# Optimization experiments

Hardware: AMD Instinct MI355X
Metric: run time of the kernel (lower is better)

## Reference

```python
import jax, jax.numpy as jnp
import numpy as np

NBLOCK = 2000
DIM = 2048
B, T = 32, 1024
EPS = 1e-12  # F.normalize eps


def _l2norm(v, axis):
    n = jnp.sqrt(jnp.sum(v * v, axis=axis, keepdims=True))
    return v / jnp.maximum(n, EPS)


def setup_inputs() -> dict:
    key = jax.random.key(0)
    kx, km, kw = jax.random.split(key, 3)
    x = jax.random.normal(kx, (B, T, DIM), dtype=jnp.float32)
    mask = jax.random.randint(km, (B, T), 0, 2).astype(jnp.int32)
    stdv = 1.0 / np.sqrt(DIM)
    weight = jax.random.uniform(kw, (NBLOCK, DIM), dtype=jnp.float32,
                                minval=-stdv, maxval=stdv)
    return {"x": x, "mask": mask, "weight": weight}


def reference(x, mask, weight):
    half = x.shape[0] // 2
    nblock = weight.shape[0]
    m = mask.astype(x.dtype)  # [B, T]

    # diversity: || W W^T - I ||_F
    gram = weight @ weight.T  # [N, N]
    diversity_loss = jnp.linalg.norm(gram - jnp.eye(nblock, dtype=weight.dtype))

    # cosine-similarity attention: [B, T, N]
    att = jnp.einsum('btd,nd->btn', _l2norm(x, axis=2), _l2norm(weight, axis=1))

    # uniformity loss: masked sum over T, softmax over blocks, mean over half-batch
    s = jnp.einsum('btn,bt->nb', att[:half], m[:half])  # [N, half]
    tmp = jnp.mean(jax.nn.softmax(s, axis=0), axis=1)   # [N]
    u_loss = jnp.linalg.norm(tmp)

    # per-row min over masked positions of the top-1 similarity
    top1 = jnp.max(att, axis=2)  # [B, T] (only topk[...,0] is used)
    inf = jnp.asarray(jnp.inf, dtype=x.dtype)
    masked_top1 = jnp.where(m > 0, top1, inf)
    min_sim = jnp.min(masked_top1[:half], axis=1)   # [half]
    ab_min = jnp.min(masked_top1[half:], axis=1)    # [half]

    return (0.2 * diversity_loss,
            2.0 - jnp.mean(min_sim) + jnp.mean(ab_min),
            0.5 * u_loss)
```

## Files before the change

kernel.cpp:

```cpp
#include <hip/hip_runtime.h>

typedef unsigned short u16;
typedef unsigned int u32;
typedef __attribute__((ext_vector_type(8))) short short8;
typedef __attribute__((ext_vector_type(8))) u16 ushort8;
typedef __attribute__((ext_vector_type(4))) u16 ushort4_t;
typedef __attribute__((ext_vector_type(4))) float fx4;

#define DIMK 2048
#define NBLK 2000

typedef const __attribute__((address_space(1))) void* gp_t;
typedef __attribute__((address_space(3))) void* lp_t;

__device__ __forceinline__ u16 f2bf(float f) {
  u32 u = __float_as_uint(f);
  u32 r = (u + 0x7fffu + ((u >> 16) & 1u)) >> 16;
  return (u16)r;
}

__device__ __forceinline__ u32 fkey(float f) {
  u32 u = __float_as_uint(f);
  return (u & 0x80000000u) ? ~u : (u | 0x80000000u);
}
__device__ __forceinline__ float dekey(u32 k) {
  u32 u = (k & 0x80000000u) ? (k ^ 0x80000000u) : ~k;
  return __uint_as_float(u);
}

__device__ __forceinline__ void ring_gemm128(const u16* gA0, const u16* gA1,
                                             const u16* gB0, const u16* gB1,
                                             u16 (*ring)[2][4096],
                                             int wv, int wr, int wc, int fIntra,
                                             fx4 acc[4][4])
{
#pragma unroll
  for (int mi = 0; mi < 4; mi++)
#pragma unroll
    for (int ni = 0; ni < 4; ni++)
      acc[mi][ni] = fx4{0.f, 0.f, 0.f, 0.f};

#define STG(kt)                                                                  \
  do {                                                                           \
    const int ko_ = (kt) << 5;                                                   \
    u16* lA_ = &ring[(kt) % 3][0][wv << 10];                                     \
    u16* lB_ = &ring[(kt) % 3][1][wv << 10];                                     \
    __builtin_amdgcn_global_load_lds((gp_t)(gA0 + ko_), (lp_t)lA_,         16, 0, 0); \
    __builtin_amdgcn_global_load_lds((gp_t)(gA1 + ko_), (lp_t)(lA_ + 512), 16, 0, 0); \
    __builtin_amdgcn_global_load_lds((gp_t)(gB0 + ko_), (lp_t)lB_,         16, 0, 0); \
    __builtin_amdgcn_global_load_lds((gp_t)(gB1 + ko_), (lp_t)(lB_ + 512), 16, 0, 0); \
  } while (0)

  STG(0);
  STG(1);

  const int NT = DIMK / 32;
#pragma unroll 1
  for (int t = 0; t < NT; ++t) {
    if (t + 2 < NT) {
      STG(t + 2);
      asm volatile("s_waitcnt vmcnt(8)" ::: "memory");
    } else if (t + 1 < NT) {
      asm volatile("s_waitcnt vmcnt(4)" ::: "memory");
    } else {
      asm volatile("s_waitcnt vmcnt(0)" ::: "memory");
    }
    __builtin_amdgcn_s_barrier();

    const u16* lAt = &ring[t % 3][0][0];
    const u16* lBt = &ring[t % 3][1][0];
    short8 af[4], bfr[4];
#pragma unroll
    for (int ni = 0; ni < 4; ni++)
      bfr[ni] = *(const short8*)(lBt + (wc * 4 + ni) * 512 + fIntra);
#pragma unroll
    for (int mi = 0; mi < 4; mi++)
      af[mi] = *(const short8*)(lAt + (wr * 4 + mi) * 512 + fIntra);

    __builtin_amdgcn_s_setprio(1);
#pragma unroll
    for (int mi = 0; mi < 4; mi++)
#pragma unroll
      for (int ni = 0; ni < 4; ni++)
        acc[mi][ni] = __builtin_amdgcn_mfma_f32_16x16x32_bf16(af[mi], bfr[ni], acc[mi][ni], 0, 0, 0);
    __builtin_amdgcn_s_setprio(0);
    __builtin_amdgcn_s_barrier();
  }
#undef STG
}

__global__ __launch_bounds__(256) void norm_rows_x(const float* __restrict__ x,
                                                   u16* __restrict__ Xn)
{
  const int wv = threadIdx.x >> 6, lane = threadIdx.x & 63;
  const int row = blockIdx.x * 4 + wv;
  const float4* xr = (const float4*)(x + (size_t)row * DIMK);
  float4 v[8];
  float ss = 0.f;
#pragma unroll
  for (int j = 0; j < 8; j++) {
    v[j] = xr[j * 64 + lane];
    ss += v[j].x*v[j].x + v[j].y*v[j].y + v[j].z*v[j].z + v[j].w*v[j].w;
  }
#pragma unroll
  for (int off = 1; off < 64; off <<= 1) ss += __shfl_xor(ss, off);
  float inv = 1.0f / fmaxf(sqrtf(ss), 1e-12f);
  ushort4_t* o = (ushort4_t*)(Xn + (size_t)row * DIMK);
#pragma unroll
  for (int j = 0; j < 8; j++) {
    ushort4_t t;
    t[0] = f2bf(v[j].x * inv); t[1] = f2bf(v[j].y * inv);
    t[2] = f2bf(v[j].z * inv); t[3] = f2bf(v[j].w * inv);
    o[j * 64 + lane] = t;
  }
}

__global__ __launch_bounds__(256) void norm_rows_w(const float* __restrict__ w,
                                                   u16* __restrict__ Wn,
                                                   u16* __restrict__ Wb)
{
  const int wv = threadIdx.x >> 6, lane = threadIdx.x & 63;
  const int row = blockIdx.x * 4 + wv;
  ushort4_t* on_ = (ushort4_t*)(Wn + (size_t)row * DIMK);
  ushort4_t* ob_ = (ushort4_t*)(Wb + (size_t)row * DIMK);
  if (row < NBLK) {
    const float4* wr_ = (const float4*)(w + (size_t)row * DIMK);
    float4 v[8];
    float ss = 0.f;
#pragma unroll
    for (int j = 0; j < 8; j++) {
      v[j] = wr_[j * 64 + lane];
      ss += v[j].x*v[j].x + v[j].y*v[j].y + v[j].z*v[j].z + v[j].w*v[j].w;
    }
#pragma unroll
    for (int off = 1; off < 64; off <<= 1) ss += __shfl_xor(ss, off);
    float inv = 1.0f / fmaxf(sqrtf(ss), 1e-12f);
#pragma unroll
    for (int j = 0; j < 8; j++) {
      ushort4_t tn, tb;
      tn[0] = f2bf(v[j].x * inv); tn[1] = f2bf(v[j].y * inv);
      tn[2] = f2bf(v[j].z * inv); tn[3] = f2bf(v[j].w * inv);
      tb[0] = f2bf(v[j].x); tb[1] = f2bf(v[j].y);
      tb[2] = f2bf(v[j].z); tb[3] = f2bf(v[j].w);
      on_[j * 64 + lane] = tn;
      ob_[j * 64 + lane] = tb;
    }
  } else {
    ushort4_t z = ushort4_t{0, 0, 0, 0};
#pragma unroll
    for (int j = 0; j < 8; j++) { on_[j * 64 + lane] = z; ob_[j * 64 + lane] = z; }
  }
}

__global__ __launch_bounds__(256) void gram_kernel(const u16* __restrict__ Wb,
                                                   float* __restrict__ divsum)
{
  const int bx = blockIdx.x, by = blockIdx.y;
  if (by > bx) return;
  __shared__ __align__(16) u16 ring[3][2][4096];
  const int tid = threadIdx.x, wv = tid >> 6, lane = tid & 63;
  const int wr = wv & 1, wc = wv >> 1, quad = lane >> 4, lc = lane & 15;
  const int i0 = by * 128, j0 = bx * 128;

  const int srow = wv * 32 + (lane >> 2);
  const int skel = (((lane & 3) ^ ((lane >> 3) & 3)) << 3);
  const u16* gA0 = Wb + (size_t)(i0 + srow) * DIMK + skel;
  const u16* gA1 = gA0 + (size_t)16 * DIMK;
  const u16* gB0 = Wb + (size_t)(j0 + srow) * DIMK + skel;
  const u16* gB1 = gB0 + (size_t)16 * DIMK;
  const int fIntra = lc * 32 + ((quad ^ ((lc >> 1) & 3)) << 3);

  fx4 acc[4][4];
  ring_gemm128(gA0, gA1, gB0, gB1, ring, wv, wr, wc, fIntra, acc);

  const float mult = (bx == by) ? 1.0f : 2.0f;
  float local = 0.f;
#pragma unroll
  for (int mi = 0; mi < 4; mi++) {
#pragma unroll
    for (int ni = 0; ni < 4; ni++) {
#pragma unroll
      for (int r = 0; r < 4; r++) {
        int i = i0 + wr * 64 + mi * 16 + quad * 4 + r;
        int j = j0 + wc * 64 + ni * 16 + lc;
        float g = acc[mi][ni][r];
        float d = (i == j && i < NBLK) ? 1.0f : 0.0f;
        float e = g - d;
        local += e * e;
      }
    }
  }
  local *= mult;
#pragma unroll
  for (int off = 1; off < 64; off <<= 1) local += __shfl_xor(local, off);
  if (lane == 0) atomicAdd(divsum, local);
}

__global__ __launch_bounds__(256, 2) void att_kernel(const u16* __restrict__ Xn,
                                                     const u16* __restrict__ Wn,
                                                     const int* __restrict__ mask,
                                                     u32* __restrict__ top1k,
                                                     float* __restrict__ s)
{
  __shared__ __align__(16) u16 ring[3][12288];

  const int orig  = blockIdx.x;
  const int xcd   = orig & 7;
  const int local = orig >> 3;
  const int yb    = xcd * 32 + ((local >> 5) << 2) + (local & 3);
  const int xb    = (local >> 2) & 7;
  const int row0 = yb << 7, col0 = xb << 8;

  const int tid = threadIdx.x, wv = tid >> 6, lane = tid & 63;
  const int wr = wv >> 1, wc = wv & 1, quad = lane >> 4, lc = lane & 15;

  const int srow = lane >> 2;
  const int skel = (((lane & 3) ^ ((lane >> 3) & 3)) << 3);
  const u16* gA0 = Xn + (size_t)(row0 + wv * 32 + srow) * DIMK + skel;
  const u16* gA1 = gA0 + (size_t)16 * DIMK;
  const u16* gB0 = Wn + (size_t)(col0 + wv * 64 + srow) * DIMK + skel;
  const u16* gB1 = gB0 + (size_t)16 * DIMK;
  const u16* gB2 = gB0 + (size_t)32 * DIMK;
  const u16* gB3 = gB0 + (size_t)48 * DIMK;
  const int fIntra = lc * 32 + ((quad ^ ((lc >> 1) & 3)) << 3);

  fx4 acc[4][8];
#pragma unroll
  for (int mi = 0; mi < 4; mi++)
#pragma unroll
    for (int ni = 0; ni < 8; ni++)
      acc[mi][ni] = fx4{0.f, 0.f, 0.f, 0.f};

#define STG6(kt)                                                                 \
  do {                                                                           \
    const int ko_ = (kt) << 5;                                                   \
    u16* lA_ = &ring[(kt) % 3][wv << 10];                                        \
    u16* lB_ = &ring[(kt) % 3][4096 + (wv << 11)];                               \
    __builtin_amdgcn_global_load_lds((gp_t)(gA0 + ko_), (lp_t)lA_,          16, 0, 0); \
    __builtin_amdgcn_global_load_lds((gp_t)(gA1 + ko_), (lp_t)(lA_ + 512),  16, 0, 0); \
    __builtin_amdgcn_global_load_lds((gp_t)(gB0 + ko_), (lp_t)lB_,          16, 0, 0); \
    __builtin_amdgcn_global_load_lds((gp_t)(gB1 + ko_), (lp_t)(lB_ + 512),  16, 0, 0); \
    __builtin_amdgcn_global_load_lds((gp_t)(gB2 + ko_), (lp_t)(lB_ + 1024), 16, 0, 0); \
    __builtin_amdgcn_global_load_lds((gp_t)(gB3 + ko_), (lp_t)(lB_ + 1536), 16, 0, 0); \
  } while (0)

  STG6(0);
  STG6(1);

  const int NT = DIMK / 32;
#pragma unroll 1
  for (int t = 0; t < NT; ++t) {
    if (t + 2 < NT) {
      STG6(t + 2);
      asm volatile("s_waitcnt vmcnt(12)" ::: "memory");
    } else if (t + 1 < NT) {
      asm volatile("s_waitcnt vmcnt(6)" ::: "memory");
    } else {
      asm volatile("s_waitcnt vmcnt(0)" ::: "memory");
    }
    __builtin_amdgcn_s_barrier();

    const u16* lAt = &ring[t % 3][0];
    const u16* lBt = &ring[t % 3][0] + 4096;
    short8 af[4], bfr[8];
#pragma unroll
    for (int ni = 0; ni < 8; ni++)
      bfr[ni] = *(const short8*)(lBt + (wc * 8 + ni) * 512 + fIntra);
#pragma unroll
    for (int mi = 0; mi < 4; mi++)
      af[mi] = *(const short8*)(lAt + (wr * 4 + mi) * 512 + fIntra);

    __builtin_amdgcn_s_setprio(1);
#pragma unroll
    for (int mi = 0; mi < 4; mi++)
#pragma unroll
      for (int ni = 0; ni < 8; ni++)
        acc[mi][ni] = __builtin_amdgcn_mfma_f32_16x16x32_bf16(af[mi], bfr[ni], acc[mi][ni], 0, 0, 0);
    __builtin_amdgcn_s_setprio(0);
    __builtin_amdgcn_s_barrier();
  }
#undef STG6

#pragma unroll
  for (int mi = 0; mi < 4; mi++) {
#pragma unroll
    for (int r = 0; r < 4; r++) {
      float v = -3.0e38f;
#pragma unroll
      for (int ni = 0; ni < 8; ni++) {
        int col = col0 + wc * 128 + ni * 16 + lc;
        float av = acc[mi][ni][r];
        v = (col < NBLK && av > v) ? av : v;
      }
      v = fmaxf(v, __shfl_xor(v, 1));
      v = fmaxf(v, __shfl_xor(v, 2));
      v = fmaxf(v, __shfl_xor(v, 4));
      v = fmaxf(v, __shfl_xor(v, 8));
      if (lc == 0) {
        int row = row0 + wr * 64 + mi * 16 + quad * 4 + r;
        atomicMax(&top1k[row], fkey(v));
      }
    }
  }

  if (yb < 128) {
    const int b = yb >> 3;
    float sv[8] = {0.f, 0.f, 0.f, 0.f, 0.f, 0.f, 0.f, 0.f};
#pragma unroll
    for (int mi = 0; mi < 4; mi++) {
#pragma unroll
      for (int r = 0; r < 4; r++) {
        float mval = (float)mask[row0 + wr * 64 + mi * 16 + quad * 4 + r];
#pragma unroll
        for (int ni = 0; ni < 8; ni++)
          sv[ni] += mval * acc[mi][ni][r];
      }
    }
#pragma unroll
    for (int ni = 0; ni < 8; ni++) {
      float v = sv[ni];
      v += __shfl_xor(v, 16);
      v += __shfl_xor(v, 32);
      int col = col0 + wc * 128 + ni * 16 + lc;
      if (quad == 0 && col < NBLK)
        atomicAdd(&s[b * 2048 + col], v);
    }
  }
}

__global__ __launch_bounds__(1024) void tail_kernel(const float* __restrict__ s,
                                                    const u32* __restrict__ top1k,
                                                    const int* __restrict__ mask,
                                                    const float* __restrict__ divsum,
                                                    float* __restrict__ out)
{
  const int tid = threadIdx.x;
  const int w = tid >> 6, lane = tid & 63;
  __shared__ float mx_s[16], ise_s[16];
  __shared__ float red[16];
  __shared__ float sMin[32];

  const float* sb = s + w * 2048;
  float mx = -3.0e38f;
  for (int n = lane; n < NBLK; n += 64) mx = fmaxf(mx, sb[n]);
#pragma unroll
  for (int off = 1; off < 64; off <<= 1) mx = fmaxf(mx, __shfl_xor(mx, off));
  float se = 0.f;
  for (int n = lane; n < NBLK; n += 64) se += expf(sb[n] - mx);
#pragma unroll
  for (int off = 1; off < 64; off <<= 1) se += __shfl_xor(se, off);
  if (lane == 0) { mx_s[w] = mx; ise_s[w] = 1.0f / (se * 16.0f); }
  __syncthreads();

  float ssq = 0.f;
  for (int n = tid; n < NBLK; n += 1024) {
    float v = 0.f;
#pragma unroll
    for (int b = 0; b < 16; b++)
      v += expf(s[b * 2048 + n] - mx_s[b]) * ise_s[b];
    ssq += v * v;
  }
#pragma unroll
  for (int off = 1; off < 64; off <<= 1) ssq += __shfl_xor(ssq, off);
  if (lane == 0) red[w] = ssq;

  const int b = tid >> 5, li = tid & 31;
  float mn = 3.0e38f;
  for (int t = li; t < 1024; t += 32) {
    int idx = b * 1024 + t;
    if (mask[idx] > 0) mn = fminf(mn, dekey(top1k[idx]));
  }
#pragma unroll
  for (int off = 1; off < 32; off <<= 1) mn = fminf(mn, __shfl_xor(mn, off));
  if (li == 0) sMin[b] = mn;
  __syncthreads();

  if (tid == 0) {
    float m0 = 0.f, m1 = 0.f;
    for (int i = 0; i < 16; i++) { m0 += sMin[i]; m1 += sMin[16 + i]; }
    m0 *= (1.0f / 16.0f); m1 *= (1.0f / 16.0f);
    float sq = 0.f;
    for (int i = 0; i < 16; i++) sq += red[i];
    out[0] = 0.2f * sqrtf(divsum[0]);
    out[1] = 2.0f - m0 + m1;
    out[2] = 0.5f * sqrtf(sq);
  }
}

extern "C" void kernel_launch(void* const* d_in, const int* in_sizes, int n_in,
                              void* d_out, int out_size, void* d_ws, size_t ws_size,
                              hipStream_t stream) {
  const float* x    = (const float*)d_in[0];
  const int*   mask = (const int*)d_in[1];
  const float* w    = (const float*)d_in[2];
  float* out = (float*)d_out;

  char* ws = (char*)d_ws;
  u32*   top1k  = (u32*)(ws);
  float* s      = (float*)(ws + 131072);
  float* divsum = (float*)(ws + 270336);
  u16*   Xn     = (u16*)(ws + 270592);
  u16*   Wn     = (u16*)(ws + 270592 + 134217728ull);
  u16*   Wb     = (u16*)(ws + 270592 + 134217728ull + 8388608ull);

  hipMemsetAsync(ws, 0, 270592, stream);

  norm_rows_w<<<dim3(512), dim3(256), 0, stream>>>(w, Wn, Wb);
  norm_rows_x<<<dim3(8192), dim3(256), 0, stream>>>(x, Xn);
  gram_kernel<<<dim3(16, 16), dim3(256), 0, stream>>>(Wb, divsum);
  att_kernel<<<dim3(2048), dim3(256), 0, stream>>>(Xn, Wn, mask, top1k, s);
  tail_kernel<<<dim3(1), dim3(1024), 0, stream>>>(s, top1k, mask, divsum, out);
}
```

Measured before the change: 724.7 us.

## Replace LDS triple-buffered staging with direct global-to-register MFMA operand loads

Both GEMM kernels (gram and attention) drop the shared-memory ring buffer fed by global_load_lds, along with its waitcnt and barrier pipeline. Each wave now loads its MFMA A/B fragments straight from global memory into registers at every k-step. This removes LDS traffic, barriers and LDS occupancy limits. In exchange it loses data sharing across waves, so the same tiles are fetched multiple times through cache, and there is no explicit prefetch, leaving global latency exposed each iteration.

Measured after the change: 1.205 ms. 66.3% more time.

```diff
diff --git a/kernel.cpp b/kernel.cpp
--- a/kernel.cpp
+++ b/kernel.cpp
@@ -3,15 +3,11 @@
 typedef unsigned short u16;
 typedef unsigned int u32;
 typedef __attribute__((ext_vector_type(8))) short short8;
-typedef __attribute__((ext_vector_type(8))) u16 ushort8;
 typedef __attribute__((ext_vector_type(4))) u16 ushort4_t;
 typedef __attribute__((ext_vector_type(4))) float fx4;
 
 #define DIMK 2048
 #define NBLK 2000
-
-typedef const __attribute__((address_space(1))) void* gp_t;
-typedef __attribute__((address_space(3))) void* lp_t;
 
 __device__ __forceinline__ u16 f2bf(float f) {
   u32 u = __float_as_uint(f);
@@ -26,67 +22,6 @@
 __device__ __forceinline__ float dekey(u32 k) {
   u32 u = (k & 0x80000000u) ? (k ^ 0x80000000u) : ~k;
   return __uint_as_float(u);
-}
-
-__device__ __forceinline__ void ring_gemm128(const u16* gA0, const u16* gA1,
-                                             const u16* gB0, const u16* gB1,
-                                             u16 (*ring)[2][4096],
-                                             int wv, int wr, int wc, int fIntra,
-                                             fx4 acc[4][4])
-{
-#pragma unroll
-  for (int mi = 0; mi < 4; mi++)
-#pragma unroll
-    for (int ni = 0; ni < 4; ni++)
-      acc[mi][ni] = fx4{0.f, 0.f, 0.f, 0.f};
-
-#define STG(kt)                                                                  \
-  do {                                                                           \
-    const int ko_ = (kt) << 5;                                                   \
-    u16* lA_ = &ring[(kt) % 3][0][wv << 10];                                     \
-    u16* lB_ = &ring[(kt) % 3][1][wv << 10];                                     \
-    __builtin_amdgcn_global_load_lds((gp_t)(gA0 + ko_), (lp_t)lA_,         16, 0, 0); \
-    __builtin_amdgcn_global_load_lds((gp_t)(gA1 + ko_), (lp_t)(lA_ + 512), 16, 0, 0); \
-    __builtin_amdgcn_global_load_lds((gp_t)(gB0 + ko_), (lp_t)lB_,         16, 0, 0); \
-    __builtin_amdgcn_global_load_lds((gp_t)(gB1 + ko_), (lp_t)(lB_ + 512), 16, 0, 0); \
-  } while (0)
-
-  STG(0);
-  STG(1);
-
-  const int NT = DIMK / 32;
-#pragma unroll 1
-  for (int t = 0; t < NT; ++t) {
-    if (t + 2 < NT) {
-      STG(t + 2);
-      asm volatile("s_waitcnt vmcnt(8)" ::: "memory");
-    } else if (t + 1 < NT) {
-      asm volatile("s_waitcnt vmcnt(4)" ::: "memory");
-    } else {
-      asm volatile("s_waitcnt vmcnt(0)" ::: "memory");
-    }
-    __builtin_amdgcn_s_barrier();
-
-    const u16* lAt = &ring[t % 3][0][0];
-    const u16* lBt = &ring[t % 3][1][0];
-    short8 af[4], bfr[4];
-#pragma unroll
-    for (int ni = 0; ni < 4; ni++)
-      bfr[ni] = *(const short8*)(lBt + (wc * 4 + ni) * 512 + fIntra);
-#pragma unroll
-    for (int mi = 0; mi < 4; mi++)
-      af[mi] = *(const short8*)(lAt + (wr * 4 + mi) * 512 + fIntra);
-
-    __builtin_amdgcn_s_setprio(1);
-#pragma unroll
-    for (int mi = 0; mi < 4; mi++)
-#pragma unroll
-      for (int ni = 0; ni < 4; ni++)
-        acc[mi][ni] = __builtin_amdgcn_mfma_f32_16x16x32_bf16(af[mi], bfr[ni], acc[mi][ni], 0, 0, 0);
-    __builtin_amdgcn_s_setprio(0);
-    __builtin_amdgcn_s_barrier();
-  }
-#undef STG
 }
 
 __global__ __launch_bounds__(256) void norm_rows_x(const float* __restrict__ x,
@@ -157,21 +92,36 @@
 {
   const int bx = blockIdx.x, by = blockIdx.y;
   if (by > bx) return;
-  __shared__ __align__(16) u16 ring[3][2][4096];
   const int tid = threadIdx.x, wv = tid >> 6, lane = tid & 63;
   const int wr = wv & 1, wc = wv >> 1, quad = lane >> 4, lc = lane & 15;
   const int i0 = by * 128, j0 = bx * 128;
 
-  const int srow = wv * 32 + (lane >> 2);
-  const int skel = (((lane & 3) ^ ((lane >> 3) & 3)) << 3);
-  const u16* gA0 = Wb + (size_t)(i0 + srow) * DIMK + skel;
-  const u16* gA1 = gA0 + (size_t)16 * DIMK;
-  const u16* gB0 = Wb + (size_t)(j0 + srow) * DIMK + skel;
-  const u16* gB1 = gB0 + (size_t)16 * DIMK;
-  const int fIntra = lc * 32 + ((quad ^ ((lc >> 1) & 3)) << 3);
+  const u16* Abase = Wb + (size_t)(i0 + wr * 64 + lc) * DIMK + quad * 8;
+  const u16* Bbase = Wb + (size_t)(j0 + wc * 64 + lc) * DIMK + quad * 8;
 
   fx4 acc[4][4];
-  ring_gemm128(gA0, gA1, gB0, gB1, ring, wv, wr, wc, fIntra, acc);
+#pragma unroll
+  for (int mi = 0; mi < 4; mi++)
+#pragma unroll
+    for (int ni = 0; ni < 4; ni++)
+      acc[mi][ni] = fx4{0.f, 0.f, 0.f, 0.f};
+
+#pragma unroll 1
+  for (int t = 0; t < DIMK / 32; ++t) {
+    const int k0 = t * 32;
+    short8 af[4], bfr[4];
+#pragma unroll
+    for (int mi = 0; mi < 4; mi++)
+      af[mi] = *(const short8*)(Abase + (size_t)mi * 16 * DIMK + k0);
+#pragma unroll
+    for (int ni = 0; ni < 4; ni++)
+      bfr[ni] = *(const short8*)(Bbase + (size_t)ni * 16 * DIMK + k0);
+#pragma unroll
+    for (int mi = 0; mi < 4; mi++)
+#pragma unroll
+      for (int ni = 0; ni < 4; ni++)
+        acc[mi][ni] = __builtin_amdgcn_mfma_f32_16x16x32_bf16(af[mi], bfr[ni], acc[mi][ni], 0, 0, 0);
+  }
 
   const float mult = (bx == by) ? 1.0f : 2.0f;
   float local = 0.f;
@@ -202,8 +152,6 @@
                                                      u32* __restrict__ top1k,
                                                      float* __restrict__ s)
 {
-  __shared__ __align__(16) u16 ring[3][12288];
-
   const int orig  = blockIdx.x;
   const int xcd   = orig & 7;
   const int local = orig >> 3;
@@ -214,15 +162,8 @@
   const int tid = threadIdx.x, wv = tid >> 6, lane = tid & 63;
   const int wr = wv >> 1, wc = wv & 1, quad = lane >> 4, lc = lane & 15;
 
-  const int srow = lane >> 2;
-  const int skel = (((lane & 3) ^ ((lane >> 3) & 3)) << 3);
-  const u16* gA0 = Xn + (size_t)(row0 + wv * 32 + srow) * DIMK + skel;
-  const u16* gA1 = gA0 + (size_t)16 * DIMK;
-  const u16* gB0 = Wn + (size_t)(col0 + wv * 64 + srow) * DIMK + skel;
-  const u16* gB1 = gB0 + (size_t)16 * DIMK;
-  const u16* gB2 = gB0 + (size_t)32 * DIMK;
-  const u16* gB3 = gB0 + (size_t)48 * DIMK;
-  const int fIntra = lc * 32 + ((quad ^ ((lc >> 1) & 3)) << 3);
+  const u16* Abase = Xn + (size_t)(row0 + wr * 64 + lc) * DIMK + quad * 8;
+  const u16* Bbase = Wn + (size_t)(col0 + wc * 128 + lc) * DIMK + quad * 8;
 
   fx4 acc[4][8];
 #pragma unroll
@@ -231,55 +172,22 @@
     for (int ni = 0; ni < 8; ni++)
       acc[mi][ni] = fx4{0.f, 0.f, 0.f, 0.f};
 
-#define STG6(kt)                                                                 \
-  do {                                                                           \
-    const int ko_ = (kt) << 5;                                                   \
-    u16* lA_ = &ring[(kt) % 3][wv << 10];                                        \
-    u16* lB_ = &ring[(kt) % 3][4096 + (wv << 11)];                               \
-    __builtin_amdgcn_global_load_lds((gp_t)(gA0 + ko_), (lp_t)lA_,          16, 0, 0); \
-    __builtin_amdgcn_global_load_lds((gp_t)(gA1 + ko_), (lp_t)(lA_ + 512),  16, 0, 0); \
-    __builtin_amdgcn_global_load_lds((gp_t)(gB0 + ko_), (lp_t)lB_,          16, 0, 0); \
-    __builtin_amdgcn_global_load_lds((gp_t)(gB1 + ko_), (lp_t)(lB_ + 512),  16, 0, 0); \
-    __builtin_amdgcn_global_load_lds((gp_t)(gB2 + ko_), (lp_t)(lB_ + 1024), 16, 0, 0); \
-    __builtin_amdgcn_global_load_lds((gp_t)(gB3 + ko_), (lp_t)(lB_ + 1536), 16, 0, 0); \
-  } while (0)
-
-  STG6(0);
-  STG6(1);
-
-  const int NT = DIMK / 32;
 #pragma unroll 1
-  for (int t = 0; t < NT; ++t) {
-    if (t + 2 < NT) {
-      STG6(t + 2);
-      asm volatile("s_waitcnt vmcnt(12)" ::: "memory");
-    } else if (t + 1 < NT) {
-      asm volatile("s_waitcnt vmcnt(6)" ::: "memory");
-    } else {
-      asm volatile("s_waitcnt vmcnt(0)" ::: "memory");
-    }
-    __builtin_amdgcn_s_barrier();
-
-    const u16* lAt = &ring[t % 3][0];
-    const u16* lBt = &ring[t % 3][0] + 4096;
+  for (int t = 0; t < DIMK / 32; ++t) {
+    const int k0 = t * 32;
     short8 af[4], bfr[8];
 #pragma unroll
+    for (int mi = 0; mi < 4; mi++)
+      af[mi] = *(const short8*)(Abase + (size_t)mi * 16 * DIMK + k0);
+#pragma unroll
     for (int ni = 0; ni < 8; ni++)
-      bfr[ni] = *(const short8*)(lBt + (wc * 8 + ni) * 512 + fIntra);
-#pragma unroll
-    for (int mi = 0; mi < 4; mi++)
-      af[mi] = *(const short8*)(lAt + (wr * 4 + mi) * 512 + fIntra);
-
-    __builtin_amdgcn_s_setprio(1);
+      bfr[ni] = *(const short8*)(Bbase + (size_t)ni * 16 * DIMK + k0);
 #pragma unroll
     for (int mi = 0; mi < 4; mi++)
 #pragma unroll
       for (int ni = 0; ni < 8; ni++)
         acc[mi][ni] = __builtin_amdgcn_mfma_f32_16x16x32_bf16(af[mi], bfr[ni], acc[mi][ni], 0, 0, 0);
-    __builtin_amdgcn_s_setprio(0);
-    __builtin_amdgcn_s_barrier();
-  }
-#undef STG6
+  }
 
 #pragma unroll
   for (int mi = 0; mi < 4; mi++) {
```
